# Kernel tuning notes

Hardware: AMD Instinct MI355X
Metric: run time of the kernel (lower is better)

The kernel has to match this reference:

```python
import jax, jax.numpy as jnp
import numpy as np

B, H, W, C = 64, 56, 56, 128
HEADS, WS, SHIFT = 4, 7, 3
HID = 4 * C
EPS = 1e-5
WS2 = WS * WS
DH = C // HEADS
# padding per torch code: [P_l, P_r, P_t, P_b] = [ws-shift, shift, ws-shift, shift]
P_L, P_R, P_T, P_B = WS - SHIFT, SHIFT, WS - SHIFT, SHIFT
_H, _W = H + P_T + P_B, W + P_L + P_R  # 63, 63


def layer_norm(x, g, b):
    mu = jnp.mean(x, axis=-1, keepdims=True)
    xc = x - mu
    var = jnp.mean(xc * xc, axis=-1, keepdims=True)
    return xc * jax.lax.rsqrt(var + EPS) * g + b


def setup_inputs() -> dict:
    key = jax.random.key(0)
    ks = jax.random.split(key, 12)
    s = 0.02
    return {
        "x": jax.random.normal(ks[0], (B, H * W, C), jnp.float32),
        "g1": jnp.ones((C,), jnp.float32),
        "b1": jnp.zeros((C,), jnp.float32),
        "spatial_w": jax.random.normal(ks[1], (HEADS, WS2, WS2), jnp.float32) * s,
        "spatial_b": jnp.zeros((HEADS, WS2), jnp.float32),
        "g2": jnp.ones((C,), jnp.float32),
        "b2": jnp.zeros((C,), jnp.float32),
        "fc1_w": jax.random.normal(ks[2], (C, HID), jnp.float32) * s,
        "fc1_b": jnp.zeros((HID,), jnp.float32),
        "fc2_w": jax.random.normal(ks[3], (HID, C), jnp.float32) * s,
        "fc2_b": jnp.zeros((C,), jnp.float32),
    }


def reference(x, g1, b1, spatial_w, spatial_b, g2, b2, fc1_w, fc1_b, fc2_w, fc2_b):
    shortcut = x
    xn = layer_norm(x, g1, b1).reshape(B, H, W, C)
    # shifted padding (shift_size > 0 branch)
    xp = jnp.pad(xn, ((0, 0), (P_T, P_B), (P_L, P_R), (0, 0)))  # (B,_H,_W,C)
    nh, nw = _H // WS, _W // WS
    # window_partition -> (B*nh*nw, WS*WS, C)
    xw = xp.reshape(B, nh, WS, nw, WS, C).transpose(0, 1, 3, 2, 4, 5).reshape(-1, WS2, C)
    # split heads: (nWB, HEADS, WS2, DH)
    xh = xw.reshape(-1, WS2, HEADS, DH).transpose(0, 2, 1, 3)
    # grouped 1x1 Conv1d == per-head token-mixing matmul over the WS2 axis
    yh = jnp.einsum("bhjd,hij->bhid", xh, spatial_w) + spatial_b[None, :, :, None]
    yw = yh.transpose(0, 2, 1, 3).reshape(-1, WS2, C)
    # window_reverse -> (B,_H,_W,C), then crop the shift padding
    y = yw.reshape(B, nh, nw, WS, WS, C).transpose(0, 1, 3, 2, 4, 5).reshape(B, _H, _W, C)
    y = y[:, P_T:_H - P_B, P_L:_W - P_R, :].reshape(B, H * W, C)
    x = shortcut + y
    # channel MLP with exact (erf) GELU as in F.gelu
    h = layer_norm(x, g2, b2)
    h = jax.nn.gelu(h @ fc1_w + fc1_b, approximate=False)
    x = x + (h @ fc2_w + fc2_b)
    return x
```

## Files before the change

kernel.cpp:

```cpp
#include <hip/hip_runtime.h>

typedef unsigned short u16;
typedef __attribute__((ext_vector_type(8))) short short8;
typedef __attribute__((ext_vector_type(4))) float floatx4;

#define NB 64
#define HH 56
#define WW_ 56
#define CC 128
#define NHEADS 4
#define WS2 49
#define PAD 4
#define HID 512

__device__ __forceinline__ float bf2f(u16 u){ return __uint_as_float(((unsigned)u)<<16); }
__device__ __forceinline__ u16 f2bf(float f){
  unsigned u = __float_as_uint(f);
  return (u16)((u + 0x7FFFu + ((u>>16)&1u)) >> 16);
}
__device__ __forceinline__ float gelu_f(float x){
  float u2 = x*(1.5957691216f + 0.0713548162f*x*x);
  return x / (1.f + __expf(-u2));
}
__device__ __forceinline__ short8 ld_frag(const u16* p){
  short8 v;
  #pragma unroll
  for (int e = 0; e < 8; e++) v[e] = (short)p[e];
  return v;
}

__global__ __launch_bounds__(256) void prep_k(
    const float* __restrict__ fc1_w, const float* __restrict__ fc2_w,
    const float* __restrict__ sw,
    u16* __restrict__ fc1_wT, u16* __restrict__ fc2_wT, u16* __restrict__ swT)
{
  int tid = blockIdx.x*256 + threadIdx.x;
  int nth = gridDim.x * 256;
  for (int idx = tid; idx < HID*CC; idx += nth) {
    int n = idx >> 7, k = idx & 127;
    fc1_wT[idx] = f2bf(fc1_w[k*HID + n]);
  }
  for (int idx = tid; idx < CC*HID; idx += nth) {
    int c = idx >> 9, h = idx & 511;
    fc2_wT[idx] = f2bf(fc2_w[h*CC + c]);
  }
  for (int idx = tid; idx < NHEADS*64*68; idx += nth) {
    int hd = idx / (64*68); int rem = idx - hd*64*68;
    int i = rem / 68, j = rem - i*68;
    swT[idx] = (i < WS2 && j < WS2) ? f2bf(sw[(hd*WS2 + i)*WS2 + j]) : (u16)0;
  }
}

__global__ __launch_bounds__(256, 2) void winmix_k(
    const float* __restrict__ x, const float* __restrict__ g1, const float* __restrict__ b1,
    const u16* __restrict__ swT, const float* __restrict__ sb,
    float* __restrict__ x2)
{
  __shared__ u16 wl[NHEADS*64*68];
  __shared__ u16 xnt[CC*66];
  __shared__ float sbl[NHEADS*WS2];
  int tid = threadIdx.x;
  int wvid = tid >> 6, lane = tid & 63;
  int ln = lane & 15, qd = lane >> 4;
  int b = blockIdx.x / 81; int wi = blockIdx.x - b*81;
  int wh = wi / 9, wwn = wi - wh*9;

  {
    const uint2* ws = (const uint2*)swT;
    uint2* wd = (uint2*)wl;
    #pragma unroll
    for (int r = 0; r < 17; r++) wd[tid + r*256] = ws[tid + r*256];
    if (tid < NHEADS*WS2) sbl[tid] = sb[tid];
  }

  float gl0 = g1[lane], gl1 = g1[lane+64];
  float bl0 = b1[lane], bl1 = b1[lane+64];
  for (int jj = wvid; jj < 64; jj += 4) {
    u16 o0 = 0, o1 = 0;
    if (jj < WS2) {
      int jr = jj / 7, jc = jj - jr*7;
      int pr = wh*7 + jr - PAD, pc = wwn*7 + jc - PAD;
      bool valid = (pr>=0) & (pr<HH) & (pc>=0) & (pc<WW_);
      float v0 = 0.f, v1 = 0.f;
      const float* px = x + ((size_t)((b*HH + pr)*WW_ + pc))*CC;
      if (valid) { v0 = px[lane]; v1 = px[lane+64]; }
      float s = v0 + v1, ss = v0*v0 + v1*v1;
      #pragma unroll
      for (int o = 32; o > 0; o >>= 1) { s += __shfl_xor(s, o); ss += __shfl_xor(ss, o); }
      float mu = s * (1.f/128.f);
      float var = ss * (1.f/128.f) - mu*mu;
      float rs = rsqrtf(var + 1e-5f);
      if (valid) {
        o0 = f2bf((v0 - mu)*rs*gl0 + bl0);
        o1 = f2bf((v1 - mu)*rs*gl1 + bl1);
      }
    }
    xnt[lane*66 + jj]      = o0;
    xnt[(lane+64)*66 + jj] = o1;
  }
  __syncthreads();

  int hd = wvid;
  const u16* wbase = wl + hd*64*68;
  short8 af[4][2];
  #pragma unroll
  for (int mt = 0; mt < 4; mt++)
    #pragma unroll
    for (int ks = 0; ks < 2; ks++)
      af[mt][ks] = ld_frag(&wbase[(mt*16 + ln)*68 + ks*32 + qd*8]);
  short8 bf_[2][2];
  #pragma unroll
  for (int nt = 0; nt < 2; nt++)
    #pragma unroll
    for (int ks = 0; ks < 2; ks++)
      bf_[nt][ks] = ld_frag(&xnt[(hd*32 + nt*16 + ln)*66 + ks*32 + qd*8]);
  floatx4 acc[4][2];
  #pragma unroll
  for (int mt = 0; mt < 4; mt++)
    #pragma unroll
    for (int nt = 0; nt < 2; nt++)
      acc[mt][nt] = (floatx4){0.f,0.f,0.f,0.f};
  #pragma unroll
  for (int ks = 0; ks < 2; ks++)
    #pragma unroll
    for (int mt = 0; mt < 4; mt++)
      #pragma unroll
      for (int nt = 0; nt < 2; nt++)
        acc[mt][nt] = __builtin_amdgcn_mfma_f32_16x16x32_bf16(af[mt][ks], bf_[nt][ks], acc[mt][nt], 0, 0, 0);

  #pragma unroll
  for (int mt = 0; mt < 4; mt++) {
    #pragma unroll
    for (int r = 0; r < 4; r++) {
      int i = mt*16 + qd*4 + r;
      if (i < WS2) {
        int ir = i / 7, ic = i - ir*7;
        int orow = wh*7 + ir - PAD, ocol = wwn*7 + ic - PAD;
        if (orow>=0 && orow<HH && ocol>=0 && ocol<WW_) {
          float sbv = sbl[hd*WS2 + i];
          size_t base = ((size_t)((b*HH + orow)*WW_ + ocol))*CC + hd*32;
          #pragma unroll
          for (int nt = 0; nt < 2; nt++) {
            int c = nt*16 + ln;
            x2[base + c] = x[base + c] + acc[mt][nt][r] + sbv;
          }
        }
      }
    }
  }
}

__global__ __launch_bounds__(256, 2) void mlp_k(
    float* __restrict__ xio,
    const float* __restrict__ g2, const float* __restrict__ b2,
    const u16* __restrict__ fc1_wT, const float* __restrict__ fc1_b,
    const u16* __restrict__ fc2_wT, const float* __restrict__ fc2_b)
{
  __shared__ __align__(16) char um[54272];
  __shared__ float sF1[HID];
  __shared__ float sF2[CC];
  u16* ALn = (u16*)um;
  u16* B1p = (u16*)um;
  u16* B2p = (u16*)(um + 17408);
  int tid = threadIdx.x;
  int wvid = tid >> 6, lane = tid & 63;
  int ln = lane & 15, qd = lane >> 4;
  int m0 = wvid*32;
  size_t tokbase = (size_t)blockIdx.x * 128;
  u16* Htp = (u16*)(um + 35840) + wvid*(32*72);

  sF1[tid] = fc1_b[tid]; sF1[tid+256] = fc1_b[tid+256];
  if (tid < CC) sF2[tid] = fc2_b[tid];

  float gl0 = g2[lane], gl1 = g2[lane+64];
  float bl0 = b2[lane], bl1 = b2[lane+64];
  for (int t = wvid; t < 128; t += 4) {
    const float* px = xio + (tokbase + t)*CC;
    float v0 = px[lane], v1 = px[lane+64];
    float s = v0+v1, ss = v0*v0+v1*v1;
    #pragma unroll
    for (int o = 32; o > 0; o >>= 1) { s += __shfl_xor(s,o); ss += __shfl_xor(ss,o); }
    float mu = s*(1.f/128.f), var = ss*(1.f/128.f) - mu*mu;
    float rs = rsqrtf(var + 1e-5f);
    ALn[t*136 + lane]      = f2bf((v0-mu)*rs*gl0 + bl0);
    ALn[t*136 + lane + 64] = f2bf((v1-mu)*rs*gl1 + bl1);
  }
  __syncthreads();

  short8 av1[2][4];
  #pragma unroll
  for (int mt = 0; mt < 2; mt++)
    #pragma unroll
    for (int ks = 0; ks < 4; ks++)
      av1[mt][ks] = ld_frag(&ALn[(m0 + mt*16 + ln)*136 + ks*32 + qd*8]);
  __syncthreads();

  const uint4* src1 = (const uint4*)fc1_wT;
  const uint4* src2 = (const uint4*)fc2_wT;
  uint4 p1[4], p2[4];
  int n1[4], q1[4], n2[4], q2[4];
  #pragma unroll
  for (int r = 0; r < 4; r++) {
    int idx = tid + r*256;
    n1[r] = idx >> 4; q1[r] = idx & 15;
    n2[r] = idx >> 3; q2[r] = idx & 7;
  }
  auto load_ch = [&](int cc){
    #pragma unroll
    for (int r = 0; r < 4; r++) {
      p1[r] = src1[(cc*64 + n1[r])*16 + q1[r]];
      p2[r] = src2[n2[r]*64 + cc*8 + q2[r]];
    }
  };
  auto store_ch = [&](){
    uint4* d1 = (uint4*)B1p; uint4* d2 = (uint4*)B2p;
    #pragma unroll
    for (int r = 0; r < 4; r++) {
      d1[n1[r]*17 + q1[r]] = p1[r];
      d2[n2[r]*9  + q2[r]] = p2[r];
    }
  };

  load_ch(0); store_ch();
  __syncthreads();

  floatx4 oacc[2][8];
  #pragma unroll
  for (int mt = 0; mt < 2; mt++)
    #pragma unroll
    for (int nt = 0; nt < 8; nt++) oacc[mt][nt] = (floatx4){0.f,0.f,0.f,0.f};

  for (int ch = 0; ch < 8; ch++) {
    if (ch < 7) load_ch(ch+1);

    floatx4 h[2][4];
    #pragma unroll
    for (int mt = 0; mt < 2; mt++)
      #pragma unroll
      for (int nt = 0; nt < 4; nt++) h[mt][nt] = (floatx4){0.f,0.f,0.f,0.f};
    #pragma unroll
    for (int nt = 0; nt < 4; nt++) {
      short8 bv[4];
      #pragma unroll
      for (int ks = 0; ks < 4; ks++)
        bv[ks] = ld_frag(&B1p[(nt*16 + ln)*136 + ks*32 + qd*8]);
      #pragma unroll
      for (int mt = 0; mt < 2; mt++)
        #pragma unroll
        for (int ks = 0; ks < 4; ks++)
          h[mt][nt] = __builtin_amdgcn_mfma_f32_16x16x32_bf16(av1[mt][ks], bv[ks], h[mt][nt], 0, 0, 0);
    }
    #pragma unroll
    for (int mt = 0; mt < 2; mt++)
      #pragma unroll
      for (int nt = 0; nt < 4; nt++) {
        float bias = sF1[ch*64 + nt*16 + ln];
        #pragma unroll
        for (int r = 0; r < 4; r++) {
          float g = gelu_f(h[mt][nt][r] + bias);
          int row = mt*16 + qd*4 + r;
          int col = nt*16 + ln;
          Htp[row*72 + (col ^ ((row & 8) << 1))] = f2bf(g);
        }
      }
    asm volatile("s_waitcnt lgkmcnt(0)" ::: "memory");

    short8 av2[2][2];
    #pragma unroll
    for (int mt = 0; mt < 2; mt++)
      #pragma unroll
      for (int ks = 0; ks < 2; ks++) {
        int rrow = mt*16 + ln;
        int kk = ks*32 + qd*8;
        av2[mt][ks] = ld_frag(&Htp[rrow*72 + (kk ^ ((rrow & 8) << 1))]);
      }
    #pragma unroll
    for (int nt = 0; nt < 8; nt++) {
      short8 bv2[2];
      #pragma unroll
      for (int ks = 0; ks < 2; ks++)
        bv2[ks] = ld_frag(&B2p[(nt*16 + ln)*72 + ks*32 + qd*8]);
      #pragma unroll
      for (int mt = 0; mt < 2; mt++)
        #pragma unroll
        for (int ks = 0; ks < 2; ks++)
          oacc[mt][nt] = __builtin_amdgcn_mfma_f32_16x16x32_bf16(av2[mt][ks], bv2[ks], oacc[mt][nt], 0, 0, 0);
    }
    __syncthreads();
    if (ch < 7) { store_ch(); __syncthreads(); }
  }

  #pragma unroll
  for (int mt = 0; mt < 2; mt++)
    #pragma unroll
    for (int r = 0; r < 4; r++) {
      size_t tok = tokbase + m0 + mt*16 + qd*4 + r;
      float* rowp = xio + tok*CC;
      #pragma unroll
      for (int nt = 0; nt < 8; nt++) {
        int n = nt*16 + ln;
        rowp[n] = rowp[n] + oacc[mt][nt][r] + sF2[n];
      }
    }
}

extern "C" void kernel_launch(void* const* d_in, const int* in_sizes, int n_in,
                              void* d_out, int out_size, void* d_ws, size_t ws_size,
                              hipStream_t stream) {
  const float* x     = (const float*)d_in[0];
  const float* g1    = (const float*)d_in[1];
  const float* b1    = (const float*)d_in[2];
  const float* sw    = (const float*)d_in[3];
  const float* sb    = (const float*)d_in[4];
  const float* g2    = (const float*)d_in[5];
  const float* b2    = (const float*)d_in[6];
  const float* fc1_w = (const float*)d_in[7];
  const float* fc1_b = (const float*)d_in[8];
  const float* fc2_w = (const float*)d_in[9];
  const float* fc2_b = (const float*)d_in[10];
  float* out = (float*)d_out;

  u16* fc1_wT = (u16*)d_ws;
  u16* fc2_wT = fc1_wT + HID*CC;
  u16* swT    = fc2_wT + CC*HID;

  prep_k<<<64, 256, 0, stream>>>(fc1_w, fc2_w, sw, fc1_wT, fc2_wT, swT);
  winmix_k<<<NB*81, 256, 0, stream>>>(x, g1, b1, swT, sb, out);
  mlp_k<<<(NB*HH*WW_)/128, 256, 0, stream>>>(out, g2, b2, fc1_wT, fc1_b, fc2_wT, fc2_b);
}
```

Baseline: 505.6 us.

## Read MLP weight fragments directly from global memory and make waves independent

The MLP kernel stops staging fc1/fc2 weight chunks through shared memory with block-wide barriers. Each wave now loads its weight fragments straight from global/L2 and keeps its own LayerNorm and hidden tile in a private LDS slice. The fc1 product is computed transposed (weights as the A operand), so GELU outputs can be packed and written as vectorized bf16 pairs. Dropping the shared staging and barriers frees LDS and allows three blocks per CU. The cost is redundant per-wave global weight traffic, which relies on cache hits.

```diff
diff --git a/kernel.cpp b/kernel.cpp
--- a/kernel.cpp
+++ b/kernel.cpp
@@ -18,6 +18,9 @@
   unsigned u = __float_as_uint(f);
   return (u16)((u + 0x7FFFu + ((u>>16)&1u)) >> 16);
 }
+__device__ __forceinline__ unsigned pk2(float a, float b){
+  return ((unsigned)f2bf(b) << 16) | (unsigned)f2bf(a);
+}
 __device__ __forceinline__ float gelu_f(float x){
   float u2 = x*(1.5957691216f + 0.0713548162f*x*x);
   return x / (1.f + __expf(-u2));
@@ -27,6 +30,9 @@
   #pragma unroll
   for (int e = 0; e < 8; e++) v[e] = (short)p[e];
   return v;
+}
+__device__ __forceinline__ short8 ld_frag_g(const u16* p){
+  return *(const short8*)p;
 }
 
 __global__ __launch_bounds__(256) void prep_k(
@@ -150,146 +156,96 @@
   }
 }
 
-__global__ __launch_bounds__(256, 2) void mlp_k(
+__global__ __launch_bounds__(256, 3) void mlp_k(
     float* __restrict__ xio,
     const float* __restrict__ g2, const float* __restrict__ b2,
     const u16* __restrict__ fc1_wT, const float* __restrict__ fc1_b,
     const u16* __restrict__ fc2_wT, const float* __restrict__ fc2_b)
 {
-  __shared__ __align__(16) char um[54272];
-  __shared__ float sF1[HID];
-  __shared__ float sF2[CC];
-  u16* ALn = (u16*)um;
-  u16* B1p = (u16*)um;
-  u16* B2p = (u16*)(um + 17408);
+  __shared__ __align__(16) char um[4*8704];
   int tid = threadIdx.x;
   int wvid = tid >> 6, lane = tid & 63;
   int ln = lane & 15, qd = lane >> 4;
   int m0 = wvid*32;
   size_t tokbase = (size_t)blockIdx.x * 128;
-  u16* Htp = (u16*)(um + 35840) + wvid*(32*72);
-
-  sF1[tid] = fc1_b[tid]; sF1[tid+256] = fc1_b[tid+256];
-  if (tid < CC) sF2[tid] = fc2_b[tid];
+  u16* ALnW = (u16*)(um + wvid*8704);
+  u16* Htp  = (u16*)(um + wvid*8704);
 
   float gl0 = g2[lane], gl1 = g2[lane+64];
   float bl0 = b2[lane], bl1 = b2[lane+64];
-  for (int t = wvid; t < 128; t += 4) {
-    const float* px = xio + (tokbase + t)*CC;
+  for (int t = 0; t < 32; ++t) {
+    const float* px = xio + (tokbase + m0 + t)*CC;
     float v0 = px[lane], v1 = px[lane+64];
     float s = v0+v1, ss = v0*v0+v1*v1;
     #pragma unroll
     for (int o = 32; o > 0; o >>= 1) { s += __shfl_xor(s,o); ss += __shfl_xor(ss,o); }
     float mu = s*(1.f/128.f), var = ss*(1.f/128.f) - mu*mu;
     float rs = rsqrtf(var + 1e-5f);
-    ALn[t*136 + lane]      = f2bf((v0-mu)*rs*gl0 + bl0);
-    ALn[t*136 + lane + 64] = f2bf((v1-mu)*rs*gl1 + bl1);
-  }
-  __syncthreads();
-
-  short8 av1[2][4];
+    ALnW[t*136 + lane]      = f2bf((v0-mu)*rs*gl0 + bl0);
+    ALnW[t*136 + lane + 64] = f2bf((v1-mu)*rs*gl1 + bl1);
+  }
+
+  short8 bv[2][4];
+  #pragma unroll
+  for (int n = 0; n < 2; n++)
+    #pragma unroll
+    for (int ks = 0; ks < 4; ks++)
+      bv[n][ks] = ld_frag(&ALnW[(n*16 + ln)*136 + ks*32 + qd*8]);
+
+  floatx4 oacc[2][8];
   #pragma unroll
   for (int mt = 0; mt < 2; mt++)
     #pragma unroll
-    for (int ks = 0; ks < 4; ks++)
-      av1[mt][ks] = ld_frag(&ALn[(m0 + mt*16 + ln)*136 + ks*32 + qd*8]);
-  __syncthreads();
-
-  const uint4* src1 = (const uint4*)fc1_wT;
-  const uint4* src2 = (const uint4*)fc2_wT;
-  uint4 p1[4], p2[4];
-  int n1[4], q1[4], n2[4], q2[4];
-  #pragma unroll
-  for (int r = 0; r < 4; r++) {
-    int idx = tid + r*256;
-    n1[r] = idx >> 4; q1[r] = idx & 15;
-    n2[r] = idx >> 3; q2[r] = idx & 7;
-  }
-  auto load_ch = [&](int cc){
-    #pragma unroll
-    for (int r = 0; r < 4; r++) {
-      p1[r] = src1[(cc*64 + n1[r])*16 + q1[r]];
-      p2[r] = src2[n2[r]*64 + cc*8 + q2[r]];
-    }
-  };
-  auto store_ch = [&](){
-    uint4* d1 = (uint4*)B1p; uint4* d2 = (uint4*)B2p;
-    #pragma unroll
-    for (int r = 0; r < 4; r++) {
-      d1[n1[r]*17 + q1[r]] = p1[r];
-      d2[n2[r]*9  + q2[r]] = p2[r];
-    }
-  };
-
-  load_ch(0); store_ch();
-  __syncthreads();
-
-  floatx4 oacc[2][8];
-  #pragma unroll
-  for (int mt = 0; mt < 2; mt++)
-    #pragma unroll
     for (int nt = 0; nt < 8; nt++) oacc[mt][nt] = (floatx4){0.f,0.f,0.f,0.f};
 
-  for (int ch = 0; ch < 8; ch++) {
-    if (ch < 7) load_ch(ch+1);
-
-    floatx4 h[2][4];
+  for (int ch = 0; ch < 8; ++ch) {
+    #pragma unroll
+    for (int kt = 0; kt < 4; ++kt) {
+      short8 aw[4];
+      #pragma unroll
+      for (int ks = 0; ks < 4; ks++)
+        aw[ks] = ld_frag_g(&fc1_wT[(size_t)(ch*64 + kt*16 + ln)*CC + ks*32 + qd*8]);
+      floatx4 h0 = (floatx4){0.f,0.f,0.f,0.f};
+      floatx4 h1 = (floatx4){0.f,0.f,0.f,0.f};
+      #pragma unroll
+      for (int ks = 0; ks < 4; ks++) {
+        h0 = __builtin_amdgcn_mfma_f32_16x16x32_bf16(aw[ks], bv[0][ks], h0, 0, 0, 0);
+        h1 = __builtin_amdgcn_mfma_f32_16x16x32_bf16(aw[ks], bv[1][ks], h1, 0, 0, 0);
+      }
+      floatx4 bias = *(const floatx4*)&fc1_b[ch*64 + kt*16 + qd*4];
+      uint2 u0, u1;
+      u0.x = pk2(gelu_f(h0[0]+bias[0]), gelu_f(h0[1]+bias[1]));
+      u0.y = pk2(gelu_f(h0[2]+bias[2]), gelu_f(h0[3]+bias[3]));
+      u1.x = pk2(gelu_f(h1[0]+bias[0]), gelu_f(h1[1]+bias[1]));
+      u1.y = pk2(gelu_f(h1[2]+bias[2]), gelu_f(h1[3]+bias[3]));
+      *(uint2*)&Htp[(     ln)*72 + kt*16 + qd*4] = u0;
+      *(uint2*)&Htp[(16 + ln)*72 + kt*16 + qd*4] = u1;
+    }
+    asm volatile("s_waitcnt lgkmcnt(0)" ::: "memory");
+
+    short8 av2[2][2];
     #pragma unroll
     for (int mt = 0; mt < 2; mt++)
       #pragma unroll
-      for (int nt = 0; nt < 4; nt++) h[mt][nt] = (floatx4){0.f,0.f,0.f,0.f};
-    #pragma unroll
-    for (int nt = 0; nt < 4; nt++) {
-      short8 bv[4];
-      #pragma unroll
-      for (int ks = 0; ks < 4; ks++)
-        bv[ks] = ld_frag(&B1p[(nt*16 + ln)*136 + ks*32 + qd*8]);
-      #pragma unroll
-      for (int mt = 0; mt < 2; mt++)
-        #pragma unroll
-        for (int ks = 0; ks < 4; ks++)
-          h[mt][nt] = __builtin_amdgcn_mfma_f32_16x16x32_bf16(av1[mt][ks], bv[ks], h[mt][nt], 0, 0, 0);
-    }
-    #pragma unroll
-    for (int mt = 0; mt < 2; mt++)
-      #pragma unroll
-      for (int nt = 0; nt < 4; nt++) {
-        float bias = sF1[ch*64 + nt*16 + ln];
-        #pragma unroll
-        for (int r = 0; r < 4; r++) {
-          float g = gelu_f(h[mt][nt][r] + bias);
-          int row = mt*16 + qd*4 + r;
-          int col = nt*16 + ln;
-          Htp[row*72 + (col ^ ((row & 8) << 1))] = f2bf(g);
-        }
-      }
-    asm volatile("s_waitcnt lgkmcnt(0)" ::: "memory");
-
-    short8 av2[2][2];
-    #pragma unroll
-    for (int mt = 0; mt < 2; mt++)
-      #pragma unroll
-      for (int ks = 0; ks < 2; ks++) {
-        int rrow = mt*16 + ln;
-        int kk = ks*32 + qd*8;
-        av2[mt][ks] = ld_frag(&Htp[rrow*72 + (kk ^ ((rrow & 8) << 1))]);
-      }
+      for (int ks = 0; ks < 2; ks++)
+        av2[mt][ks] = ld_frag(&Htp[(mt*16 + ln)*72 + ks*32 + qd*8]);
     #pragma unroll
     for (int nt = 0; nt < 8; nt++) {
       short8 bv2[2];
       #pragma unroll
       for (int ks = 0; ks < 2; ks++)
-        bv2[ks] = ld_frag(&B2p[(nt*16 + ln)*72 + ks*32 + qd*8]);
+        bv2[ks] = ld_frag_g(&fc2_wT[(size_t)(nt*16 + ln)*HID + ch*64 + ks*32 + qd*8]);
       #pragma unroll
       for (int mt = 0; mt < 2; mt++)
         #pragma unroll
         for (int ks = 0; ks < 2; ks++)
           oacc[mt][nt] = __builtin_amdgcn_mfma_f32_16x16x32_bf16(av2[mt][ks], bv2[ks], oacc[mt][nt], 0, 0, 0);
     }
-    __syncthreads();
-    if (ch < 7) { store_ch(); __syncthreads(); }
-  }
-
+  }
+
+  float bias2[8];
+  #pragma unroll
+  for (int nt = 0; nt < 8; nt++) bias2[nt] = fc2_b[nt*16 + ln];
   #pragma unroll
   for (int mt = 0; mt < 2; mt++)
     #pragma unroll
@@ -299,7 +255,7 @@
       #pragma unroll
       for (int nt = 0; nt < 8; nt++) {
         int n = nt*16 + ln;
-        rowp[n] = rowp[n] + oacc[mt][nt][r] + sF2[n];
+        rowp[n] = rowp[n] + oacc[mt][nt][r] + bias2[nt];
       }
     }
 }
```

Measured after the change: 549.4 us. 1.09x slower.

## Load window-mix weights directly into registers and vectorize LayerNorm loads

Applied to the files above, without the earlier changes.

The window-mixing kernel no longer stages the per-head mixing weights and biases in shared memory. Each wave loads its weight fragments straight from global memory into registers as 16-byte vectors, using a padded 80-wide row layout so those loads stay aligned. The smaller shared-memory footprint lets launch bounds rise to four blocks per CU for more occupancy. Both LayerNorms now read float2 per lane, and the MLP writes packed bf16 pairs; GELU uses a hardware reciprocal instead of a divide. The costs are repeated global/L2 weight reads per block and bias reads from global memory in the epilogue.

```diff
diff --git a/kernel.cpp b/kernel.cpp
--- a/kernel.cpp
+++ b/kernel.cpp
@@ -18,15 +18,21 @@
   unsigned u = __float_as_uint(f);
   return (u16)((u + 0x7FFFu + ((u>>16)&1u)) >> 16);
 }
+__device__ __forceinline__ unsigned pk2(float a, float b){
+  return ((unsigned)f2bf(b) << 16) | (unsigned)f2bf(a);
+}
 __device__ __forceinline__ float gelu_f(float x){
   float u2 = x*(1.5957691216f + 0.0713548162f*x*x);
-  return x / (1.f + __expf(-u2));
+  return x * __builtin_amdgcn_rcpf(1.f + __expf(-u2));
 }
 __device__ __forceinline__ short8 ld_frag(const u16* p){
   short8 v;
   #pragma unroll
   for (int e = 0; e < 8; e++) v[e] = (short)p[e];
   return v;
+}
+__device__ __forceinline__ short8 ld_frag_g(const u16* p){
+  return *(const short8*)p;
 }
 
 __global__ __launch_bounds__(256) void prep_k(
@@ -44,70 +50,60 @@
     int c = idx >> 9, h = idx & 511;
     fc2_wT[idx] = f2bf(fc2_w[h*CC + c]);
   }
-  for (int idx = tid; idx < NHEADS*64*68; idx += nth) {
-    int hd = idx / (64*68); int rem = idx - hd*64*68;
-    int i = rem / 68, j = rem - i*68;
+  for (int idx = tid; idx < NHEADS*64*80; idx += nth) {
+    int hd = idx / (64*80); int rem = idx - hd*64*80;
+    int i = rem / 80, j = rem - i*80;
     swT[idx] = (i < WS2 && j < WS2) ? f2bf(sw[(hd*WS2 + i)*WS2 + j]) : (u16)0;
   }
 }
 
-__global__ __launch_bounds__(256, 2) void winmix_k(
+__global__ __launch_bounds__(256, 4) void winmix_k(
     const float* __restrict__ x, const float* __restrict__ g1, const float* __restrict__ b1,
     const u16* __restrict__ swT, const float* __restrict__ sb,
     float* __restrict__ x2)
 {
-  __shared__ u16 wl[NHEADS*64*68];
   __shared__ u16 xnt[CC*66];
-  __shared__ float sbl[NHEADS*WS2];
   int tid = threadIdx.x;
   int wvid = tid >> 6, lane = tid & 63;
   int ln = lane & 15, qd = lane >> 4;
   int b = blockIdx.x / 81; int wi = blockIdx.x - b*81;
   int wh = wi / 9, wwn = wi - wh*9;
-
-  {
-    const uint2* ws = (const uint2*)swT;
-    uint2* wd = (uint2*)wl;
-    #pragma unroll
-    for (int r = 0; r < 17; r++) wd[tid + r*256] = ws[tid + r*256];
-    if (tid < NHEADS*WS2) sbl[tid] = sb[tid];
-  }
-
-  float gl0 = g1[lane], gl1 = g1[lane+64];
-  float bl0 = b1[lane], bl1 = b1[lane+64];
+  int hd = wvid;
+
+  short8 af[4][2];
+  #pragma unroll
+  for (int mt = 0; mt < 4; mt++)
+    #pragma unroll
+    for (int ks = 0; ks < 2; ks++)
+      af[mt][ks] = ld_frag_g(&swT[(size_t)(hd*64 + mt*16 + ln)*80 + ks*32 + qd*8]);
+
+  float2 gl = *(const float2*)&g1[2*lane];
+  float2 bl = *(const float2*)&b1[2*lane];
   for (int jj = wvid; jj < 64; jj += 4) {
     u16 o0 = 0, o1 = 0;
     if (jj < WS2) {
       int jr = jj / 7, jc = jj - jr*7;
       int pr = wh*7 + jr - PAD, pc = wwn*7 + jc - PAD;
       bool valid = (pr>=0) & (pr<HH) & (pc>=0) & (pc<WW_);
-      float v0 = 0.f, v1 = 0.f;
+      float2 v = {0.f, 0.f};
       const float* px = x + ((size_t)((b*HH + pr)*WW_ + pc))*CC;
-      if (valid) { v0 = px[lane]; v1 = px[lane+64]; }
-      float s = v0 + v1, ss = v0*v0 + v1*v1;
+      if (valid) v = *(const float2*)(px + 2*lane);
+      float s = v.x + v.y, ss = v.x*v.x + v.y*v.y;
       #pragma unroll
       for (int o = 32; o > 0; o >>= 1) { s += __shfl_xor(s, o); ss += __shfl_xor(ss, o); }
       float mu = s * (1.f/128.f);
       float var = ss * (1.f/128.f) - mu*mu;
       float rs = rsqrtf(var + 1e-5f);
       if (valid) {
-        o0 = f2bf((v0 - mu)*rs*gl0 + bl0);
-        o1 = f2bf((v1 - mu)*rs*gl1 + bl1);
-      }
-    }
-    xnt[lane*66 + jj]      = o0;
-    xnt[(lane+64)*66 + jj] = o1;
+        o0 = f2bf((v.x - mu)*rs*gl.x + bl.x);
+        o1 = f2bf((v.y - mu)*rs*gl.y + bl.y);
+      }
+    }
+    xnt[(2*lane  )*66 + jj] = o0;
+    xnt[(2*lane+1)*66 + jj] = o1;
   }
   __syncthreads();
 
-  int hd = wvid;
-  const u16* wbase = wl + hd*64*68;
-  short8 af[4][2];
-  #pragma unroll
-  for (int mt = 0; mt < 4; mt++)
-    #pragma unroll
-    for (int ks = 0; ks < 2; ks++)
-      af[mt][ks] = ld_frag(&wbase[(mt*16 + ln)*68 + ks*32 + qd*8]);
   short8 bf_[2][2];
   #pragma unroll
   for (int nt = 0; nt < 2; nt++)
@@ -137,7 +133,7 @@
         int ir = i / 7, ic = i - ir*7;
         int orow = wh*7 + ir - PAD, ocol = wwn*7 + ic - PAD;
         if (orow>=0 && orow<HH && ocol>=0 && ocol<WW_) {
-          float sbv = sbl[hd*WS2 + i];
+          float sbv = sb[hd*WS2 + i];
           size_t base = ((size_t)((b*HH + orow)*WW_ + ocol))*CC + hd*32;
           #pragma unroll
           for (int nt = 0; nt < 2; nt++) {
@@ -172,18 +168,17 @@
   sF1[tid] = fc1_b[tid]; sF1[tid+256] = fc1_b[tid+256];
   if (tid < CC) sF2[tid] = fc2_b[tid];
 
-  float gl0 = g2[lane], gl1 = g2[lane+64];
-  float bl0 = b2[lane], bl1 = b2[lane+64];
+  float2 gl = *(const float2*)&g2[2*lane];
+  float2 bl = *(const float2*)&b2[2*lane];
   for (int t = wvid; t < 128; t += 4) {
-    const float* px = xio + (tokbase + t)*CC;
-    float v0 = px[lane], v1 = px[lane+64];
-    float s = v0+v1, ss = v0*v0+v1*v1;
+    float2 v = *(const float2*)(xio + (tokbase + t)*CC + 2*lane);
+    float s = v.x + v.y, ss = v.x*v.x + v.y*v.y;
     #pragma unroll
     for (int o = 32; o > 0; o >>= 1) { s += __shfl_xor(s,o); ss += __shfl_xor(ss,o); }
     float mu = s*(1.f/128.f), var = ss*(1.f/128.f) - mu*mu;
     float rs = rsqrtf(var + 1e-5f);
-    ALn[t*136 + lane]      = f2bf((v0-mu)*rs*gl0 + bl0);
-    ALn[t*136 + lane + 64] = f2bf((v1-mu)*rs*gl1 + bl1);
+    *(unsigned*)&ALn[t*136 + 2*lane] =
+        pk2((v.x-mu)*rs*gl.x + bl.x, (v.y-mu)*rs*gl.y + bl.y);
   }
   __syncthreads();
 
```

Measured after the change: 459.9 us. 1.1x faster.
